# Kernel tuning notes

Measured on AMD Instinct MI355X. Metric: run time of the kernel, lower is better.

Reference implementation:

```python
import jax, jax.numpy as jnp
import numpy as np

# samplelist: node i -> output nodes (2i, 2i+1); flattened index is identity.
SAMPLELIST = [(2 * i, 2 * i + 1) for i in range(32)]
INDEX = np.array([j for t in SAMPLELIST for j in t])  # scatter: out[..., INDEX[i]] = cat[..., i]
INV = np.argsort(INDEX)  # equivalent gather permutation

B, CIN, COUT, F, N, K = 128, 16, 16, 512, 32, 2


def setup_inputs() -> dict:
    key = jax.random.key(0)
    ks = jax.random.split(key, 5)
    x = jax.random.normal(ks[0], (B, CIN, F, N), dtype=jnp.float32)
    # ConvTranspose2d weight layout [in, out, 1, kw] -> stacked per node [N, Cin, Cout, K]
    W1 = jax.random.normal(ks[1], (N, CIN, COUT, K), dtype=jnp.float32) * 0.1
    b1 = jax.random.normal(ks[2], (N, COUT), dtype=jnp.float32) * 0.1
    W2 = jax.random.normal(ks[3], (N, COUT, COUT), dtype=jnp.float32) * 0.1  # 1x1 convT
    b2 = jax.random.normal(ks[4], (N, COUT), dtype=jnp.float32) * 0.1
    return {"x": x, "W1": W1, "b1": b1, "W2": W2, "b2": b2}


def reference(x, W1, b1, W2, b2):
    # Per-node ConvTranspose2d with kernel (1,K) on a single-node slice is a
    # channel contraction that fans node n out to K output positions.
    # y1: [B, Cout, F, N, K]
    y1 = jnp.einsum('bifn,niok->bofnk', x, W1) + b1.T[None, :, None, :, None]
    # Second ConvTranspose2d is 1x1: pure per-node channel mix.
    y2 = jnp.einsum('bofnk,noc->bcfnk', y1, W2) + b2.T[None, :, None, :, None]
    y = y2.reshape(B, COUT, F, N * K)  # concat over node dim, matching torch.cat
    # Reorder columns: out[..., INDEX[i]] = y[..., i]  <=>  gather with INV.
    return jnp.take(y, jnp.asarray(INV), axis=3)
```

## Files before the change

### kernel.cpp

```cpp
#include <hip/hip_runtime.h>

#define B_    128
#define CIN_  16
#define COUT_ 16
#define F_    512
#define N_    32
#define FC    16

typedef float f32x2 __attribute__((ext_vector_type(2)));

__global__ __launch_bounds__(256) void weff_kernel(
    const float* __restrict__ W1, const float* __restrict__ b1,
    const float* __restrict__ W2, const float* __restrict__ b2,
    float* __restrict__ Weff, float* __restrict__ beff) {
  const int t = blockIdx.x * 256 + threadIdx.x;
  const int n = t >> 8, c = (t >> 4) & 15, i = t & 15;
  const float* w1 = W1 + (size_t)((n * 16 + i) * 16) * 2;
  const float* w2 = W2 + (size_t)(n * 16) * 16 + c;
  float a0 = 0.f, a1 = 0.f;
#pragma unroll
  for (int o = 0; o < 16; ++o) {
    const float m = w2[o * 16];
    a0 += w1[o * 2 + 0] * m;
    a1 += w1[o * 2 + 1] * m;
  }
  Weff[(size_t)((n * 16 + c) * 16 + i) * 2 + 0] = a0;
  Weff[(size_t)((n * 16 + c) * 16 + i) * 2 + 1] = a1;
  if (t < 512) {
    const int nn = t >> 4, cc = t & 15;
    float s = b2[nn * 16 + cc];
#pragma unroll
    for (int o = 0; o < 16; ++o)
      s += b1[nn * 16 + o] * W2[(nn * 16 + o) * 16 + cc];
    beff[t] = s;
  }
}

__global__ __launch_bounds__(256) void up_kernel(
    const float* __restrict__ x, const float* __restrict__ Weff,
    const float* __restrict__ beff, float* __restrict__ out) {
  __shared__ float4 xs4[4 * FC * 32];

  const int bid = blockIdx.x;
  const int b   = bid >> 5;
  const int f0  = (bid & 31) * FC;
  const int t   = threadIdx.x;

#pragma unroll
  for (int s = 0; s < 2; ++s) {
    const int q  = t + 256 * s;
    const int g  = q >> 7;
    const int df = (q >> 3) & 15;
    const int n4 = q & 7;
    const float* src =
        x + ((size_t)(b * CIN_ + 4 * g) * F_ + (f0 + df)) * N_ + n4 * 4;
    const float4 v0 = *(const float4*)(src + 0 * (size_t)F_ * N_);
    const float4 v1 = *(const float4*)(src + 1 * (size_t)F_ * N_);
    const float4 v2 = *(const float4*)(src + 2 * (size_t)F_ * N_);
    const float4 v3 = *(const float4*)(src + 3 * (size_t)F_ * N_);
    const int u0  = (g * FC + df) * 32 + n4 * 4;
    const int key = df & 7;
    xs4[(u0 + 0) ^ key] = make_float4(v0.x, v1.x, v2.x, v3.x);
    xs4[(u0 + 1) ^ key] = make_float4(v0.y, v1.y, v2.y, v3.y);
    xs4[(u0 + 2) ^ key] = make_float4(v0.z, v1.z, v2.z, v3.z);
    xs4[(u0 + 3) ^ key] = make_float4(v0.w, v1.w, v2.w, v3.w);
  }

  const int n  = t & 31;
  const int cg = t >> 5;
  float w[2][32];
  float bias[2];
#pragma unroll
  for (int cc = 0; cc < 2; ++cc) {
    const int c = cg + cc * 8;
    const float4* wp = (const float4*)(Weff + (size_t)(n * 16 + c) * 32);
#pragma unroll
    for (int j = 0; j < 8; ++j) {
      const float4 v = wp[j];
      w[cc][4 * j + 0] = v.x;
      w[cc][4 * j + 1] = v.y;
      w[cc][4 * j + 2] = v.z;
      w[cc][4 * j + 3] = v.w;
    }
    bias[cc] = beff[n * 16 + c];
  }

  __syncthreads();

  float* o0 = out + ((size_t)(b * COUT_ + cg) * F_ + f0) * 64 + 2 * n;
  float* o1 = o0 + (size_t)8 * F_ * 64;

#pragma unroll 4
  for (int df = 0; df < FC; ++df) {
    float a00 = bias[0], a01 = bias[0];
    float a10 = bias[1], a11 = bias[1];
#pragma unroll
    for (int g = 0; g < 4; ++g) {
      const float4 xv = xs4[((g * FC + df) * 32 + n) ^ (df & 7)];
      const float xi[4] = {xv.x, xv.y, xv.z, xv.w};
#pragma unroll
      for (int r = 0; r < 4; ++r) {
        const int i = 4 * g + r;
        a00 += xi[r] * w[0][2 * i + 0];
        a01 += xi[r] * w[0][2 * i + 1];
        a10 += xi[r] * w[1][2 * i + 0];
        a11 += xi[r] * w[1][2 * i + 1];
      }
    }
    f32x2 r0; r0.x = a00; r0.y = a01;
    f32x2 r1; r1.x = a10; r1.y = a11;
    __builtin_nontemporal_store(r0, (f32x2*)(o0 + df * 64));
    __builtin_nontemporal_store(r1, (f32x2*)(o1 + df * 64));
  }
}

extern "C" void kernel_launch(void* const* d_in, const int* in_sizes, int n_in,
                              void* d_out, int out_size, void* d_ws, size_t ws_size,
                              hipStream_t stream) {
  const float* x  = (const float*)d_in[0];
  const float* W1 = (const float*)d_in[1];
  const float* b1 = (const float*)d_in[2];
  const float* W2 = (const float*)d_in[3];
  const float* b2 = (const float*)d_in[4];
  float* out = (float*)d_out;

  float* Weff = (float*)d_ws;
  float* beff = Weff + N_ * COUT_ * CIN_ * 2;

  weff_kernel<<<32, 256, 0, stream>>>(W1, b1, W2, b2, Weff, beff);
  up_kernel<<<B_ * (F_ / FC), 256, 0, stream>>>(x, Weff, beff, out);
}
```

Before: 366.9 us.

## Split x tile into two halves and prefetch second half during first compute

Splits each block's 16-row slice of x into two 8-row halves held in a double-buffered shared array. The second half's global loads are issued into registers before the first half is computed, so their latency is hidden behind compute and stores. This adds a second barrier and more live registers per thread. The overall memory traffic is unchanged.

```diff
diff --git a/kernel.cpp b/kernel.cpp
--- a/kernel.cpp
+++ b/kernel.cpp
@@ -6,6 +6,7 @@
 #define F_    512
 #define N_    32
 #define FC    16
+#define FS    8
 
 typedef float f32x2 __attribute__((ext_vector_type(2)));
 
@@ -39,32 +40,23 @@
 __global__ __launch_bounds__(256) void up_kernel(
     const float* __restrict__ x, const float* __restrict__ Weff,
     const float* __restrict__ beff, float* __restrict__ out) {
-  __shared__ float4 xs4[4 * FC * 32];
+  __shared__ float4 xs4[2][4 * FS * 32];
 
   const int bid = blockIdx.x;
   const int b   = bid >> 5;
   const int f0  = (bid & 31) * FC;
   const int t   = threadIdx.x;
 
-#pragma unroll
-  for (int s = 0; s < 2; ++s) {
-    const int q  = t + 256 * s;
-    const int g  = q >> 7;
-    const int df = (q >> 3) & 15;
-    const int n4 = q & 7;
-    const float* src =
-        x + ((size_t)(b * CIN_ + 4 * g) * F_ + (f0 + df)) * N_ + n4 * 4;
-    const float4 v0 = *(const float4*)(src + 0 * (size_t)F_ * N_);
-    const float4 v1 = *(const float4*)(src + 1 * (size_t)F_ * N_);
-    const float4 v2 = *(const float4*)(src + 2 * (size_t)F_ * N_);
-    const float4 v3 = *(const float4*)(src + 3 * (size_t)F_ * N_);
-    const int u0  = (g * FC + df) * 32 + n4 * 4;
-    const int key = df & 7;
-    xs4[(u0 + 0) ^ key] = make_float4(v0.x, v1.x, v2.x, v3.x);
-    xs4[(u0 + 1) ^ key] = make_float4(v0.y, v1.y, v2.y, v3.y);
-    xs4[(u0 + 2) ^ key] = make_float4(v0.z, v1.z, v2.z, v3.z);
-    xs4[(u0 + 3) ^ key] = make_float4(v0.w, v1.w, v2.w, v3.w);
-  }
+  const int g   = t >> 6;
+  const int dfq = (t >> 3) & 7;
+  const int n4  = t & 7;
+  const float* src =
+      x + ((size_t)(b * CIN_ + 4 * g) * F_ + (f0 + dfq)) * N_ + n4 * 4;
+
+  float4 v0 = *(const float4*)(src + 0 * (size_t)F_ * N_);
+  float4 v1 = *(const float4*)(src + 1 * (size_t)F_ * N_);
+  float4 v2 = *(const float4*)(src + 2 * (size_t)F_ * N_);
+  float4 v3 = *(const float4*)(src + 3 * (size_t)F_ * N_);
 
   const int n  = t & 31;
   const int cg = t >> 5;
@@ -85,22 +77,35 @@
     bias[cc] = beff[n * 16 + c];
   }
 
+  const int u0  = (g * FS + dfq) * 32 + n4 * 4;
+  const int key = dfq;
+
+  xs4[0][(u0 + 0) ^ key] = make_float4(v0.x, v1.x, v2.x, v3.x);
+  xs4[0][(u0 + 1) ^ key] = make_float4(v0.y, v1.y, v2.y, v3.y);
+  xs4[0][(u0 + 2) ^ key] = make_float4(v0.z, v1.z, v2.z, v3.z);
+  xs4[0][(u0 + 3) ^ key] = make_float4(v0.w, v1.w, v2.w, v3.w);
+
+  v0 = *(const float4*)(src + 0 * (size_t)F_ * N_ + FS * N_);
+  v1 = *(const float4*)(src + 1 * (size_t)F_ * N_ + FS * N_);
+  v2 = *(const float4*)(src + 2 * (size_t)F_ * N_ + FS * N_);
+  v3 = *(const float4*)(src + 3 * (size_t)F_ * N_ + FS * N_);
+
   __syncthreads();
 
   float* o0 = out + ((size_t)(b * COUT_ + cg) * F_ + f0) * 64 + 2 * n;
   float* o1 = o0 + (size_t)8 * F_ * 64;
 
 #pragma unroll 4
-  for (int df = 0; df < FC; ++df) {
+  for (int df = 0; df < FS; ++df) {
     float a00 = bias[0], a01 = bias[0];
     float a10 = bias[1], a11 = bias[1];
 #pragma unroll
-    for (int g = 0; g < 4; ++g) {
-      const float4 xv = xs4[((g * FC + df) * 32 + n) ^ (df & 7)];
+    for (int gg = 0; gg < 4; ++gg) {
+      const float4 xv = xs4[0][((gg * FS + df) * 32 + n) ^ df];
       const float xi[4] = {xv.x, xv.y, xv.z, xv.w};
 #pragma unroll
       for (int r = 0; r < 4; ++r) {
-        const int i = 4 * g + r;
+        const int i = 4 * gg + r;
         a00 += xi[r] * w[0][2 * i + 0];
         a01 += xi[r] * w[0][2 * i + 1];
         a10 += xi[r] * w[1][2 * i + 0];
@@ -111,6 +116,36 @@
     f32x2 r1; r1.x = a10; r1.y = a11;
     __builtin_nontemporal_store(r0, (f32x2*)(o0 + df * 64));
     __builtin_nontemporal_store(r1, (f32x2*)(o1 + df * 64));
+  }
+
+  xs4[1][(u0 + 0) ^ key] = make_float4(v0.x, v1.x, v2.x, v3.x);
+  xs4[1][(u0 + 1) ^ key] = make_float4(v0.y, v1.y, v2.y, v3.y);
+  xs4[1][(u0 + 2) ^ key] = make_float4(v0.z, v1.z, v2.z, v3.z);
+  xs4[1][(u0 + 3) ^ key] = make_float4(v0.w, v1.w, v2.w, v3.w);
+
+  __syncthreads();
+
+#pragma unroll 4
+  for (int df = 0; df < FS; ++df) {
+    float a00 = bias[0], a01 = bias[0];
+    float a10 = bias[1], a11 = bias[1];
+#pragma unroll
+    for (int gg = 0; gg < 4; ++gg) {
+      const float4 xv = xs4[1][((gg * FS + df) * 32 + n) ^ df];
+      const float xi[4] = {xv.x, xv.y, xv.z, xv.w};
+#pragma unroll
+      for (int r = 0; r < 4; ++r) {
+        const int i = 4 * gg + r;
+        a00 += xi[r] * w[0][2 * i + 0];
+        a01 += xi[r] * w[0][2 * i + 1];
+        a10 += xi[r] * w[1][2 * i + 0];
+        a11 += xi[r] * w[1][2 * i + 1];
+      }
+    }
+    f32x2 r0; r0.x = a00; r0.y = a01;
+    f32x2 r1; r1.x = a10; r1.y = a11;
+    __builtin_nontemporal_store(r0, (f32x2*)(o0 + (FS + df) * 64));
+    __builtin_nontemporal_store(r1, (f32x2*)(o1 + (FS + df) * 64));
   }
 }
 
```

Result: no change. 370.8 us (+1.1%).
